# Optimization experiments

Hardware: AMD Instinct MI355X
Metric: run time of the kernel (lower is better)

## Reference

```python
import jax, jax.numpy as jnp
import numpy as np

N = 50000      # nodes (full graph: num_dst == num_src == N)
E = 800000     # edges, avg degree 16
D = 128        # in_feats == n_hidden == out_feats
L = 3          # n_layers
EPS = 1e-5     # BatchNorm1d eps


def setup_inputs() -> dict:
    key = jax.random.key(0)
    ks = jax.random.split(key, 6)
    feat = jax.random.normal(ks[0], (N, D), dtype=jnp.float32)
    src = jax.random.randint(ks[1], (E,), 0, N)
    dst = jax.random.randint(ks[2], (E,), 0, N)
    scale = 1.0 / np.sqrt(D)
    W_self = jax.random.normal(ks[3], (L, D, D), dtype=jnp.float32) * scale
    W_neigh = jax.random.normal(ks[4], (L, D, D), dtype=jnp.float32) * scale
    b = jax.random.normal(ks[5], (L, D), dtype=jnp.float32) * 0.01
    gamma = jnp.ones((L - 1, D), dtype=jnp.float32)
    beta = jnp.zeros((L - 1, D), dtype=jnp.float32)
    return {"feat": feat, "src": src, "dst": dst, "W_self": W_self,
            "W_neigh": W_neigh, "b": b, "gamma": gamma, "beta": beta}


def reference(feat, src, dst, W_self, W_neigh, b, gamma, beta):
    n = feat.shape[0]
    n_layers = W_self.shape[0]
    # in-degree of each dst node, clamped to 1 (zero-degree nodes aggregate 0)
    deg = jax.ops.segment_sum(jnp.ones_like(dst, dtype=feat.dtype), dst,
                              num_segments=n)
    deg = jnp.maximum(deg, 1.0)[:, None]                      # [N,1]
    h = feat
    for i in range(n_layers):
        # mean aggregation over incoming neighbors: gather + segment-sum
        agg = jax.ops.segment_sum(h[src], dst, num_segments=n) / deg  # [N,D]
        # SAGEConv('mean'): fc_self(h_dst) + fc_neigh(agg) + bias
        hn = h @ W_self[i] + agg @ W_neigh[i] + b[i]
        hn = hn + h                                           # residual (dims match)
        if i < n_layers - 1:
            mu = jnp.mean(hn, axis=0)
            var = jnp.var(hn, axis=0)                         # biased, as BN training
            hn = (hn - mu) * jax.lax.rsqrt(var + EPS) * gamma[i] + beta[i]
            hn = jax.nn.relu(hn)
        h = hn
    return h
```

## Files before the change

### kernel.cpp

```cpp
#include <hip/hip_runtime.h>

#define DIM 128
#define EPSF 1e-5f
#define BK_SHIFT 8
#define BK_NODES 256
#define GRP_SHIFT 13
#define NGRP 8
#define BKS_CAP 1536
#define MAXNBS 1600

typedef __attribute__((ext_vector_type(8))) short short8;
typedef __attribute__((ext_vector_type(4))) float float4v;

__device__ inline unsigned short f2bf(float x) {
    union { float f; unsigned u; } z; z.f = x;
    unsigned u = z.u;
    unsigned r = u + 0x7FFF + ((u >> 16) & 1);
    return (unsigned short)(r >> 16);
}
__device__ inline float bf2f(unsigned short u) {
    union { unsigned u; float f; } z; z.u = ((unsigned)u) << 16;
    return z.f;
}

__global__ void binA_kernel(const int* __restrict__ src, const int* __restrict__ dst,
                            unsigned* __restrict__ barr, int* __restrict__ bcnt,
                            int E, int NBS) {
    __shared__ int cnt[MAXNBS];
    __shared__ int gcur[MAXNBS];
    int tid = threadIdx.x;
    int tile0 = blockIdx.x * 4096;
    for (int j = tid; j < NBS; j += 256) cnt[j] = 0;
    __syncthreads();
    unsigned pk[16]; int bk[16];
#pragma unroll
    for (int i = 0; i < 16; ++i) {
        int e = tile0 + i * 256 + tid;
        if (e < E) {
            int d = dst[e];
            int s = src[e];
            bk[i] = ((d >> BK_SHIFT) << 3) | (s >> GRP_SHIFT);
            pk[i] = ((unsigned)(d & (BK_NODES - 1)) << 16) | (unsigned)s;
            atomicAdd(&cnt[bk[i]], 1);
        } else bk[i] = -1;
    }
    __syncthreads();
    for (int j = tid; j < NBS; j += 256) {
        int c = cnt[j];
        gcur[j] = (c > 0) ? atomicAdd(&bcnt[j], c) : 0;
    }
    __syncthreads();
#pragma unroll
    for (int i = 0; i < 16; ++i) {
        if (bk[i] >= 0) {
            int pos = atomicAdd(&gcur[bk[i]], 1);
            if (pos < BKS_CAP)
                barr[(size_t)bk[i] * BKS_CAP + pos] = pk[i];
        }
    }
}

__global__ void binB_kernel(const unsigned* __restrict__ barr, const int* __restrict__ bcnt,
                            int* __restrict__ rowptr, int* __restrict__ colidx,
                            int N, int E, int NBS) {
    __shared__ int hist[256];
    __shared__ int sm[256];
    __shared__ int bc[NGRP];
    int b = blockIdx.x;
    int tid = threadIdx.x;
    int lim = b * NGRP;
    int part = 0;
    for (int i = tid; i < lim; i += 256) part += bcnt[i];
    sm[tid] = part;
    if (tid < NGRP) bc[tid] = bcnt[lim + tid];
    __syncthreads();
    for (int off = 128; off > 0; off >>= 1) {
        if (tid < off) sm[tid] += sm[tid + off];
        __syncthreads();
    }
    int gb = sm[0];
    if (b == 0 && tid == 0) rowptr[N] = E;
    __syncthreads();
    hist[tid] = 0;
    __syncthreads();
    for (int g = 0; g < NGRP; ++g) {
        int cg = bc[g]; if (cg > BKS_CAP) cg = BKS_CAP;
        const unsigned* arr = barr + (size_t)(b * NGRP + g) * BKS_CAP;
        for (int i = tid; i < cg; i += 256)
            atomicAdd(&hist[arr[i] >> 16], 1);
    }
    __syncthreads();
    int h = hist[tid];
    sm[tid] = h;
    __syncthreads();
    for (int off = 1; off < 256; off <<= 1) {
        int x = (tid >= off) ? sm[tid - off] : 0;
        __syncthreads();
        sm[tid] += x;
        __syncthreads();
    }
    int base = sm[tid] - h;
    hist[tid] = base;
    int node = (b << BK_SHIFT) + tid;
    if (node < N) rowptr[node] = gb + base;
    __syncthreads();
    for (int g = 0; g < NGRP; ++g) {
        int cg = bc[g]; if (cg > BKS_CAP) cg = BKS_CAP;
        const unsigned* arr = barr + (size_t)(b * NGRP + g) * BKS_CAP;
        for (int i = tid; i < cg; i += 256) {
            unsigned u = arr[i];
            int pos = atomicAdd(&hist[u >> 16], 1);
            colidx[gb + pos] = (int)(u & 0xFFFFu);
        }
        __syncthreads();
    }
}

__global__ void prep_kernel(const float* __restrict__ Ws, const float* __restrict__ Wn,
                            unsigned short* __restrict__ wpack,
                            const float* __restrict__ feat, unsigned short* __restrict__ Hd,
                            int N) {
    int b = blockIdx.x;
    int tid = threadIdx.x;
    if (b < 24) {
        int l = b >> 3;
        int s = b & 7;
#pragma unroll
        for (int pi = 0; pi < 2; ++pi) {
            int p = tid * 2 + pi;
            int nt = p >> 6;
            int lane = p & 63;
            int kb = s * 32 + (lane >> 4) * 8;
            int col = nt * 16 + (lane & 15);
            unsigned short* dstp = wpack + (size_t)l * 32768 + ((size_t)(s * 8 + nt) * 64 + lane) * 8;
#pragma unroll
            for (int j = 0; j < 8; ++j) {
                int k = kb + j;
                float v = (k < 128) ? Ws[(size_t)l * 16384 + k * 128 + col]
                                    : Wn[(size_t)l * 16384 + (k - 128) * 128 + col];
                dstp[j] = f2bf(v);
            }
        }
        return;
    }
    int idx = (b - 24) * 256 + tid;
    if (idx >= N * 32) return;
    float4 v = ((const float4*)feat)[idx];
    ushort4 o;
    o.x = f2bf(v.x); o.y = f2bf(v.y); o.z = f2bf(v.z); o.w = f2bf(v.w);
    ((ushort4*)Hd)[idx] = o;
}

template<int BN>
__global__ void aggregate_kernel(const unsigned short* __restrict__ Hd,
                                 unsigned short* __restrict__ Acat,
                                 const int* __restrict__ rowptr,
                                 const int* __restrict__ colidx,
                                 const float* __restrict__ stats,
                                 const float* __restrict__ gamma,
                                 const float* __restrict__ beta,
                                 float invN, int N) {
    int wid = (blockIdx.x * blockDim.x + threadIdx.x) >> 6;
    if (wid >= N) return;
    int lane = threadIdx.x & 63;
    int half = lane >> 5, sl = lane & 31;
    float sc[4], sh[4];
    if (BN) {
#pragma unroll
        for (int j = 0; j < 4; ++j) {
            int c = sl * 4 + j;
            float mean = stats[c] * invN;
            float var = stats[128 + c] * invN - mean * mean;
            float s = gamma[c] * rsqrtf(var + EPSF);
            sc[j] = s; sh[j] = beta[c] - mean * s;
        }
    }
#define BNOP0(x) fmaxf(fmaf(bf2f(x), sc[0], sh[0]), 0.f)
#define BNOP1(x) fmaxf(fmaf(bf2f(x), sc[1], sh[1]), 0.f)
#define BNOP2(x) fmaxf(fmaf(bf2f(x), sc[2], sh[2]), 0.f)
#define BNOP3(x) fmaxf(fmaf(bf2f(x), sc[3], sh[3]), 0.f)
    int beg = rowptr[wid], end = rowptr[wid + 1];
    float4 acc = make_float4(0.f, 0.f, 0.f, 0.f);
    int e = beg + half;
    for (; e + 6 < end; e += 8) {
        int s0 = colidx[e];
        int s1 = colidx[e + 2];
        int s2 = colidx[e + 4];
        int s3 = colidx[e + 6];
        ushort4 u0 = *(const ushort4*)(Hd + (size_t)s0 * 128 + sl * 4);
        ushort4 u1 = *(const ushort4*)(Hd + (size_t)s1 * 128 + sl * 4);
        ushort4 u2 = *(const ushort4*)(Hd + (size_t)s2 * 128 + sl * 4);
        ushort4 u3 = *(const ushort4*)(Hd + (size_t)s3 * 128 + sl * 4);
        if (BN) {
            acc.x += (BNOP0(u0.x) + BNOP0(u1.x)) + (BNOP0(u2.x) + BNOP0(u3.x));
            acc.y += (BNOP1(u0.y) + BNOP1(u1.y)) + (BNOP1(u2.y) + BNOP1(u3.y));
            acc.z += (BNOP2(u0.z) + BNOP2(u1.z)) + (BNOP2(u2.z) + BNOP2(u3.z));
            acc.w += (BNOP3(u0.w) + BNOP3(u1.w)) + (BNOP3(u2.w) + BNOP3(u3.w));
        } else {
            acc.x += (bf2f(u0.x) + bf2f(u1.x)) + (bf2f(u2.x) + bf2f(u3.x));
            acc.y += (bf2f(u0.y) + bf2f(u1.y)) + (bf2f(u2.y) + bf2f(u3.y));
            acc.z += (bf2f(u0.z) + bf2f(u1.z)) + (bf2f(u2.z) + bf2f(u3.z));
            acc.w += (bf2f(u0.w) + bf2f(u1.w)) + (bf2f(u2.w) + bf2f(u3.w));
        }
    }
    for (; e < end; e += 2) {
        int s0 = colidx[e];
        ushort4 u0 = *(const ushort4*)(Hd + (size_t)s0 * 128 + sl * 4);
        if (BN) {
            acc.x += BNOP0(u0.x);
            acc.y += BNOP1(u0.y);
            acc.z += BNOP2(u0.z);
            acc.w += BNOP3(u0.w);
        } else {
            acc.x += bf2f(u0.x);
            acc.y += bf2f(u0.y);
            acc.z += bf2f(u0.z);
            acc.w += bf2f(u0.w);
        }
    }
    acc.x += __shfl_xor(acc.x, 32);
    acc.y += __shfl_xor(acc.y, 32);
    acc.z += __shfl_xor(acc.z, 32);
    acc.w += __shfl_xor(acc.w, 32);
    if (half == 0) {
        int deg = end - beg;
        float inv = 1.0f / (float)(deg > 0 ? deg : 1);
        ushort4 hrow = *(const ushort4*)(Hd + (size_t)wid * 128 + sl * 4);
        ushort4 ho;
        if (BN) {
            ho.x = f2bf(BNOP0(hrow.x));
            ho.y = f2bf(BNOP1(hrow.y));
            ho.z = f2bf(BNOP2(hrow.z));
            ho.w = f2bf(BNOP3(hrow.w));
        } else ho = hrow;
        *(ushort4*)(Acat + (size_t)wid * 256 + sl * 4) = ho;
        ushort4 o;
        o.x = f2bf(acc.x * inv); o.y = f2bf(acc.y * inv);
        o.z = f2bf(acc.z * inv); o.w = f2bf(acc.w * inv);
        *(ushort4*)(Acat + (size_t)wid * 256 + 128 + sl * 4) = o;
    }
#undef BNOP0
#undef BNOP1
#undef BNOP2
#undef BNOP3
}

__launch_bounds__(256)
__global__ void gemm_kernel(const unsigned short* __restrict__ Acat,
                            const unsigned short* __restrict__ wpack,
                            const float* __restrict__ bias,
                            unsigned short* __restrict__ outb, float* __restrict__ outf,
                            float* __restrict__ stats, int withStats, int N) {
    __shared__ unsigned short Bs[32768];
    int tid = threadIdx.x;
    {
        const float4* wsrc = (const float4*)wpack;
        float4* bdst = (float4*)Bs;
#pragma unroll
        for (int i = 0; i < 16; ++i) bdst[i * 256 + tid] = wsrc[i * 256 + tid];
    }
    __syncthreads();

    int wave = tid >> 6, lane = tid & 63;
    int row0 = blockIdx.x * 128 + wave * 32;
    int mrow = lane & 15, kq = lane >> 4;
    const unsigned short* Abase = Acat + (size_t)(row0 + mrow) * 256 + kq * 8;

    float4v acc[2][8];
#pragma unroll
    for (int i = 0; i < 2; ++i)
#pragma unroll
        for (int j = 0; j < 8; ++j) acc[i][j] = (float4v){0.f, 0.f, 0.f, 0.f};

#pragma unroll
    for (int s = 0; s < 8; ++s) {
        short8 a0 = *(const short8*)(Abase + s * 32);
        short8 a1 = *(const short8*)(Abase + 16 * 256 + s * 32);
#pragma unroll
        for (int nt = 0; nt < 8; ++nt) {
            short8 b = *(const short8*)(Bs + ((size_t)(s * 8 + nt) * 64 + lane) * 8);
            acc[0][nt] = __builtin_amdgcn_mfma_f32_16x16x32_bf16(a0, b, acc[0][nt], 0, 0, 0);
            acc[1][nt] = __builtin_amdgcn_mfma_f32_16x16x32_bf16(a1, b, acc[1][nt], 0, 0, 0);
        }
    }

    float* sm = (float*)Bs;
    if (withStats) {
        __syncthreads();
        sm[tid] = 0.f;
        __syncthreads();
    }

    int colb = lane & 15;
    int rq = (lane >> 4) * 4;
#pragma unroll
    for (int mt = 0; mt < 2; ++mt) {
        int rowt = row0 + mt * 16 + rq;
#pragma unroll
        for (int nt = 0; nt < 8; ++nt) {
            int col = nt * 16 + colb;
            float bv = bias[col];
            float slo = 0.f, qlo = 0.f;
#pragma unroll
            for (int r = 0; r < 4; ++r) {
                int row = rowt + r;
                if (row < N) {
                    float res = bf2f(Acat[(size_t)row * 256 + col]);
                    float v = acc[mt][nt][r] + bv + res;
                    if (withStats) {
                        outb[(size_t)row * 128 + col] = f2bf(v);
                        slo += v; qlo += v * v;
                    } else {
                        outf[(size_t)row * 128 + col] = v;
                    }
                }
            }
            if (withStats) {
                atomicAdd(&sm[col], slo);
                atomicAdd(&sm[128 + col], qlo);
            }
        }
    }
    if (withStats) {
        __syncthreads();
        if (tid < 128) {
            atomicAdd(&stats[tid], sm[tid]);
            atomicAdd(&stats[128 + tid], sm[128 + tid]);
        }
    }
}

extern "C" void kernel_launch(void* const* d_in, const int* in_sizes, int n_in,
                              void* d_out, int out_size, void* d_ws, size_t ws_size,
                              hipStream_t stream) {
    const float* feat  = (const float*)d_in[0];
    const int*   src   = (const int*)d_in[1];
    const int*   dst   = (const int*)d_in[2];
    const float* Wself = (const float*)d_in[3];
    const float* Wneig = (const float*)d_in[4];
    const float* bias  = (const float*)d_in[5];
    const float* gamma = (const float*)d_in[6];
    const float* beta  = (const float*)d_in[7];

    int N = in_sizes[0] / DIM;
    int E = in_sizes[1];
    int Npad = (N + 127) & ~127;
    int NB = (N + BK_NODES - 1) >> BK_SHIFT;
    int NBS = NB * NGRP;

    char* ws = (char*)d_ws;
    size_t off = 0;
    auto alloc = [&](size_t bytes) -> void* {
        void* p = ws + off;
        off = (off + bytes + 255) & ~(size_t)255;
        return p;
    };
    unsigned short* Acat   = (unsigned short*)alloc((size_t)Npad * 256 * 2);
    unsigned short* Hd     = (unsigned short*)alloc((size_t)Npad * 128 * 2);
    unsigned short* wpack  = (unsigned short*)alloc((size_t)3 * 32768 * 2);
    int*   colidx = (int*)alloc((size_t)E * 4);
    int*   rowptr = (int*)alloc((size_t)(N + 1) * 4);
    int*   bcnt   = (int*)alloc(MAXNBS * 4);
    float* stats  = (float*)alloc(512 * 4);

    unsigned* barr = (unsigned*)Acat;

    hipMemsetAsync(bcnt, 0, MAXNBS * 4 + 512 * 4, stream);
    binA_kernel<<<(E + 4095) / 4096, 256, 0, stream>>>(src, dst, barr, bcnt, E, NBS);
    binB_kernel<<<NB, 256, 0, stream>>>(barr, bcnt, rowptr, colidx, N, E, NBS);

    prep_kernel<<<24 + (N * 32 + 255) / 256, 256, 0, stream>>>(Wself, Wneig, wpack, feat, Hd, N);

    float invN = 1.0f / (float)N;
    int nagg = (N + 3) / 4;

    aggregate_kernel<0><<<nagg, 256, 0, stream>>>(Hd, Acat, rowptr, colidx,
                                                  stats, gamma, beta, invN, N);
    gemm_kernel<<<Npad / 128, 256, 0, stream>>>(Acat, wpack, bias, Hd, (float*)d_out,
                                                stats, 1, N);
    aggregate_kernel<1><<<nagg, 256, 0, stream>>>(Hd, Acat, rowptr, colidx,
                                                  stats, gamma, beta, invN, N);
    gemm_kernel<<<Npad / 128, 256, 0, stream>>>(Acat, wpack + 32768, bias + DIM, Hd,
                                                (float*)d_out, stats + 256, 1, N);
    aggregate_kernel<1><<<nagg, 256, 0, stream>>>(Hd, Acat, rowptr, colidx,
                                                  stats + 256, gamma + DIM, beta + DIM, invN, N);
    gemm_kernel<<<Npad / 128, 256, 0, stream>>>(Acat, wpack + 2 * 32768, bias + 2 * DIM, Hd,
                                                (float*)d_out, stats, 0, N);
}
```

Measured before the change: 325.5 us.

## Fuse all three layers into one persistent cooperative kernel with grid syncs

Replaces the six per-layer aggregate and GEMM launches with a single cooperative persistent kernel that loops over layers and separates phases with grid-wide syncs. BatchNorm+ReLU now runs as a separate elementwise pass that writes a normalized bf16 buffer, instead of being applied on every gathered neighbour. The GEMM reads self and aggregated features from two separate buffers rather than one concatenated array, and streams weights from global memory instead of staging them in LDS. This removes launch gaps and repeated per-edge BN arithmetic, but adds grid-sync costs, an extra full pass over H per layer, and lower occupancy under the persistent grid.

```diff
diff --git a/kernel.cpp b/kernel.cpp
--- a/kernel.cpp
+++ b/kernel.cpp
@@ -1,4 +1,7 @@
 #include <hip/hip_runtime.h>
+#include <hip/hip_cooperative_groups.h>
+
+namespace cg = cooperative_groups;
 
 #define DIM 128
 #define EPSF 1e-5f
@@ -118,7 +121,7 @@
 
 __global__ void prep_kernel(const float* __restrict__ Ws, const float* __restrict__ Wn,
                             unsigned short* __restrict__ wpack,
-                            const float* __restrict__ feat, unsigned short* __restrict__ Hd,
+                            const float* __restrict__ feat, unsigned short* __restrict__ Hb,
                             int N) {
     int b = blockIdx.x;
     int tid = threadIdx.x;
@@ -148,185 +151,176 @@
     float4 v = ((const float4*)feat)[idx];
     ushort4 o;
     o.x = f2bf(v.x); o.y = f2bf(v.y); o.z = f2bf(v.z); o.w = f2bf(v.w);
-    ((ushort4*)Hd)[idx] = o;
-}
-
-template<int BN>
-__global__ void aggregate_kernel(const unsigned short* __restrict__ Hd,
-                                 unsigned short* __restrict__ Acat,
-                                 const int* __restrict__ rowptr,
-                                 const int* __restrict__ colidx,
-                                 const float* __restrict__ stats,
-                                 const float* __restrict__ gamma,
-                                 const float* __restrict__ beta,
-                                 float invN, int N) {
-    int wid = (blockIdx.x * blockDim.x + threadIdx.x) >> 6;
-    if (wid >= N) return;
-    int lane = threadIdx.x & 63;
-    int half = lane >> 5, sl = lane & 31;
-    float sc[4], sh[4];
-    if (BN) {
-#pragma unroll
-        for (int j = 0; j < 4; ++j) {
-            int c = sl * 4 + j;
-            float mean = stats[c] * invN;
-            float var = stats[128 + c] * invN - mean * mean;
-            float s = gamma[c] * rsqrtf(var + EPSF);
-            sc[j] = s; sh[j] = beta[c] - mean * s;
-        }
-    }
-#define BNOP0(x) fmaxf(fmaf(bf2f(x), sc[0], sh[0]), 0.f)
-#define BNOP1(x) fmaxf(fmaf(bf2f(x), sc[1], sh[1]), 0.f)
-#define BNOP2(x) fmaxf(fmaf(bf2f(x), sc[2], sh[2]), 0.f)
-#define BNOP3(x) fmaxf(fmaf(bf2f(x), sc[3], sh[3]), 0.f)
-    int beg = rowptr[wid], end = rowptr[wid + 1];
-    float4 acc = make_float4(0.f, 0.f, 0.f, 0.f);
-    int e = beg + half;
-    for (; e + 6 < end; e += 8) {
-        int s0 = colidx[e];
-        int s1 = colidx[e + 2];
-        int s2 = colidx[e + 4];
-        int s3 = colidx[e + 6];
-        ushort4 u0 = *(const ushort4*)(Hd + (size_t)s0 * 128 + sl * 4);
-        ushort4 u1 = *(const ushort4*)(Hd + (size_t)s1 * 128 + sl * 4);
-        ushort4 u2 = *(const ushort4*)(Hd + (size_t)s2 * 128 + sl * 4);
-        ushort4 u3 = *(const ushort4*)(Hd + (size_t)s3 * 128 + sl * 4);
-        if (BN) {
-            acc.x += (BNOP0(u0.x) + BNOP0(u1.x)) + (BNOP0(u2.x) + BNOP0(u3.x));
-            acc.y += (BNOP1(u0.y) + BNOP1(u1.y)) + (BNOP1(u2.y) + BNOP1(u3.y));
-            acc.z += (BNOP2(u0.z) + BNOP2(u1.z)) + (BNOP2(u2.z) + BNOP2(u3.z));
-            acc.w += (BNOP3(u0.w) + BNOP3(u1.w)) + (BNOP3(u2.w) + BNOP3(u3.w));
-        } else {
-            acc.x += (bf2f(u0.x) + bf2f(u1.x)) + (bf2f(u2.x) + bf2f(u3.x));
-            acc.y += (bf2f(u0.y) + bf2f(u1.y)) + (bf2f(u2.y) + bf2f(u3.y));
-            acc.z += (bf2f(u0.z) + bf2f(u1.z)) + (bf2f(u2.z) + bf2f(u3.z));
-            acc.w += (bf2f(u0.w) + bf2f(u1.w)) + (bf2f(u2.w) + bf2f(u3.w));
-        }
-    }
-    for (; e < end; e += 2) {
-        int s0 = colidx[e];
-        ushort4 u0 = *(const ushort4*)(Hd + (size_t)s0 * 128 + sl * 4);
-        if (BN) {
-            acc.x += BNOP0(u0.x);
-            acc.y += BNOP1(u0.y);
-            acc.z += BNOP2(u0.z);
-            acc.w += BNOP3(u0.w);
-        } else {
-            acc.x += bf2f(u0.x);
-            acc.y += bf2f(u0.y);
-            acc.z += bf2f(u0.z);
-            acc.w += bf2f(u0.w);
-        }
-    }
-    acc.x += __shfl_xor(acc.x, 32);
-    acc.y += __shfl_xor(acc.y, 32);
-    acc.z += __shfl_xor(acc.z, 32);
-    acc.w += __shfl_xor(acc.w, 32);
-    if (half == 0) {
-        int deg = end - beg;
-        float inv = 1.0f / (float)(deg > 0 ? deg : 1);
-        ushort4 hrow = *(const ushort4*)(Hd + (size_t)wid * 128 + sl * 4);
-        ushort4 ho;
-        if (BN) {
-            ho.x = f2bf(BNOP0(hrow.x));
-            ho.y = f2bf(BNOP1(hrow.y));
-            ho.z = f2bf(BNOP2(hrow.z));
-            ho.w = f2bf(BNOP3(hrow.w));
-        } else ho = hrow;
-        *(ushort4*)(Acat + (size_t)wid * 256 + sl * 4) = ho;
-        ushort4 o;
-        o.x = f2bf(acc.x * inv); o.y = f2bf(acc.y * inv);
-        o.z = f2bf(acc.z * inv); o.w = f2bf(acc.w * inv);
-        *(ushort4*)(Acat + (size_t)wid * 256 + 128 + sl * 4) = o;
-    }
-#undef BNOP0
-#undef BNOP1
-#undef BNOP2
-#undef BNOP3
-}
-
-__launch_bounds__(256)
-__global__ void gemm_kernel(const unsigned short* __restrict__ Acat,
-                            const unsigned short* __restrict__ wpack,
-                            const float* __restrict__ bias,
-                            unsigned short* __restrict__ outb, float* __restrict__ outf,
-                            float* __restrict__ stats, int withStats, int N) {
-    __shared__ unsigned short Bs[32768];
-    int tid = threadIdx.x;
-    {
-        const float4* wsrc = (const float4*)wpack;
-        float4* bdst = (float4*)Bs;
-#pragma unroll
-        for (int i = 0; i < 16; ++i) bdst[i * 256 + tid] = wsrc[i * 256 + tid];
-    }
-    __syncthreads();
-
-    int wave = tid >> 6, lane = tid & 63;
-    int row0 = blockIdx.x * 128 + wave * 32;
-    int mrow = lane & 15, kq = lane >> 4;
-    const unsigned short* Abase = Acat + (size_t)(row0 + mrow) * 256 + kq * 8;
-
-    float4v acc[2][8];
-#pragma unroll
-    for (int i = 0; i < 2; ++i)
-#pragma unroll
-        for (int j = 0; j < 8; ++j) acc[i][j] = (float4v){0.f, 0.f, 0.f, 0.f};
-
-#pragma unroll
-    for (int s = 0; s < 8; ++s) {
-        short8 a0 = *(const short8*)(Abase + s * 32);
-        short8 a1 = *(const short8*)(Abase + 16 * 256 + s * 32);
-#pragma unroll
-        for (int nt = 0; nt < 8; ++nt) {
-            short8 b = *(const short8*)(Bs + ((size_t)(s * 8 + nt) * 64 + lane) * 8);
-            acc[0][nt] = __builtin_amdgcn_mfma_f32_16x16x32_bf16(a0, b, acc[0][nt], 0, 0, 0);
-            acc[1][nt] = __builtin_amdgcn_mfma_f32_16x16x32_bf16(a1, b, acc[1][nt], 0, 0, 0);
-        }
-    }
-
-    float* sm = (float*)Bs;
-    if (withStats) {
-        __syncthreads();
-        sm[tid] = 0.f;
-        __syncthreads();
-    }
-
-    int colb = lane & 15;
-    int rq = (lane >> 4) * 4;
-#pragma unroll
-    for (int mt = 0; mt < 2; ++mt) {
-        int rowt = row0 + mt * 16 + rq;
-#pragma unroll
-        for (int nt = 0; nt < 8; ++nt) {
-            int col = nt * 16 + colb;
-            float bv = bias[col];
-            float slo = 0.f, qlo = 0.f;
-#pragma unroll
-            for (int r = 0; r < 4; ++r) {
-                int row = rowt + r;
-                if (row < N) {
-                    float res = bf2f(Acat[(size_t)row * 256 + col]);
-                    float v = acc[mt][nt][r] + bv + res;
-                    if (withStats) {
-                        outb[(size_t)row * 128 + col] = f2bf(v);
-                        slo += v; qlo += v * v;
-                    } else {
-                        outf[(size_t)row * 128 + col] = v;
+    ((ushort4*)Hb)[idx] = o;
+}
+
+__launch_bounds__(256, 4)
+__global__ void layers_kernel(unsigned short* __restrict__ Hb,
+                              unsigned short* __restrict__ Agg,
+                              unsigned short* __restrict__ Hd,
+                              const int* __restrict__ rowptr,
+                              const int* __restrict__ colidx,
+                              const unsigned short* __restrict__ wpack,
+                              const float* __restrict__ bias,
+                              const float* __restrict__ gamma,
+                              const float* __restrict__ beta,
+                              float* __restrict__ stats,
+                              float* __restrict__ outf,
+                              float invN, int N, int Npad) {
+    cg::grid_group grid = cg::this_grid();
+    __shared__ float sm[256];
+    const int tid = threadIdx.x;
+    const int gthreads = gridDim.x * 256;
+    const int lane = tid & 63;
+
+    for (int l = 0; l < 3; ++l) {
+        if (l > 0) {
+            const volatile float* st = stats + (size_t)(l - 1) * 256;
+            int idx0 = blockIdx.x * 256 + tid;
+            int c0 = (idx0 & 31) * 4;
+            float sc[4], sh[4];
+#pragma unroll
+            for (int j = 0; j < 4; ++j) {
+                float mean = st[c0 + j] * invN;
+                float var = st[128 + c0 + j] * invN - mean * mean;
+                float s = gamma[(size_t)(l - 1) * DIM + c0 + j] * rsqrtf(var + EPSF);
+                sc[j] = s;
+                sh[j] = beta[(size_t)(l - 1) * DIM + c0 + j] - mean * s;
+            }
+            for (int idx = idx0; idx < N * 32; idx += gthreads) {
+                ushort4 u = ((const ushort4*)Hd)[idx];
+                ushort4 o;
+                o.x = f2bf(fmaxf(fmaf(bf2f(u.x), sc[0], sh[0]), 0.f));
+                o.y = f2bf(fmaxf(fmaf(bf2f(u.y), sc[1], sh[1]), 0.f));
+                o.z = f2bf(fmaxf(fmaf(bf2f(u.z), sc[2], sh[2]), 0.f));
+                o.w = f2bf(fmaxf(fmaf(bf2f(u.w), sc[3], sh[3]), 0.f));
+                ((ushort4*)Hb)[idx] = o;
+            }
+            grid.sync();
+        }
+
+        {
+            int gw = (blockIdx.x * 256 + tid) >> 6;
+            int nw = gthreads >> 6;
+            int half = lane >> 5, sl = lane & 31;
+            for (int wid = gw; wid < N; wid += nw) {
+                int beg = rowptr[wid], end = rowptr[wid + 1];
+                float4 acc = make_float4(0.f, 0.f, 0.f, 0.f);
+                int e = beg + half;
+                for (; e + 6 < end; e += 8) {
+                    int s0 = colidx[e];
+                    int s1 = colidx[e + 2];
+                    int s2 = colidx[e + 4];
+                    int s3 = colidx[e + 6];
+                    ushort4 u0 = *(const ushort4*)(Hb + (size_t)s0 * 128 + sl * 4);
+                    ushort4 u1 = *(const ushort4*)(Hb + (size_t)s1 * 128 + sl * 4);
+                    ushort4 u2 = *(const ushort4*)(Hb + (size_t)s2 * 128 + sl * 4);
+                    ushort4 u3 = *(const ushort4*)(Hb + (size_t)s3 * 128 + sl * 4);
+                    acc.x += (bf2f(u0.x) + bf2f(u1.x)) + (bf2f(u2.x) + bf2f(u3.x));
+                    acc.y += (bf2f(u0.y) + bf2f(u1.y)) + (bf2f(u2.y) + bf2f(u3.y));
+                    acc.z += (bf2f(u0.z) + bf2f(u1.z)) + (bf2f(u2.z) + bf2f(u3.z));
+                    acc.w += (bf2f(u0.w) + bf2f(u1.w)) + (bf2f(u2.w) + bf2f(u3.w));
+                }
+                for (; e < end; e += 2) {
+                    int s0 = colidx[e];
+                    ushort4 u0 = *(const ushort4*)(Hb + (size_t)s0 * 128 + sl * 4);
+                    acc.x += bf2f(u0.x);
+                    acc.y += bf2f(u0.y);
+                    acc.z += bf2f(u0.z);
+                    acc.w += bf2f(u0.w);
+                }
+                acc.x += __shfl_xor(acc.x, 32);
+                acc.y += __shfl_xor(acc.y, 32);
+                acc.z += __shfl_xor(acc.z, 32);
+                acc.w += __shfl_xor(acc.w, 32);
+                if (half == 0) {
+                    int deg = end - beg;
+                    float inv = 1.0f / (float)(deg > 0 ? deg : 1);
+                    ushort4 o;
+                    o.x = f2bf(acc.x * inv); o.y = f2bf(acc.y * inv);
+                    o.z = f2bf(acc.z * inv); o.w = f2bf(acc.w * inv);
+                    *(ushort4*)(Agg + (size_t)wid * 128 + sl * 4) = o;
+                }
+            }
+        }
+        grid.sync();
+
+        {
+            const unsigned short* wl = wpack + (size_t)l * 32768;
+            int withStats = (l < 2) ? 1 : 0;
+            int ntile = Npad >> 7;
+            int wave = tid >> 6;
+            int mrow = lane & 15, kq = lane >> 4;
+            for (int t = blockIdx.x; t < ntile; t += gridDim.x) {
+                int row0 = t * 128 + wave * 32;
+                const unsigned short* Sbase = Hb + (size_t)(row0 + mrow) * 128 + kq * 8;
+                const unsigned short* Gbase = Agg + (size_t)(row0 + mrow) * 128 + kq * 8;
+
+                float4v acc[2][8];
+#pragma unroll
+                for (int i = 0; i < 2; ++i)
+#pragma unroll
+                    for (int j = 0; j < 8; ++j) acc[i][j] = (float4v){0.f, 0.f, 0.f, 0.f};
+
+#pragma unroll
+                for (int s = 0; s < 8; ++s) {
+                    const unsigned short* ab = (s < 4) ? (Sbase + s * 32)
+                                                       : (Gbase + (s - 4) * 32);
+                    short8 a0 = *(const short8*)ab;
+                    short8 a1 = *(const short8*)(ab + 16 * 128);
+#pragma unroll
+                    for (int nt = 0; nt < 8; ++nt) {
+                        short8 b = *(const short8*)(wl + ((size_t)(s * 8 + nt) * 64 + lane) * 8);
+                        acc[0][nt] = __builtin_amdgcn_mfma_f32_16x16x32_bf16(a0, b, acc[0][nt], 0, 0, 0);
+                        acc[1][nt] = __builtin_amdgcn_mfma_f32_16x16x32_bf16(a1, b, acc[1][nt], 0, 0, 0);
                     }
                 }
-            }
-            if (withStats) {
-                atomicAdd(&sm[col], slo);
-                atomicAdd(&sm[128 + col], qlo);
-            }
-        }
-    }
-    if (withStats) {
-        __syncthreads();
-        if (tid < 128) {
-            atomicAdd(&stats[tid], sm[tid]);
-            atomicAdd(&stats[128 + tid], sm[128 + tid]);
-        }
+
+                if (withStats) {
+                    __syncthreads();
+                    sm[tid] = 0.f;
+                    __syncthreads();
+                }
+                int colb = lane & 15;
+                int rq = (lane >> 4) * 4;
+#pragma unroll
+                for (int mt = 0; mt < 2; ++mt) {
+                    int rowt = row0 + mt * 16 + rq;
+#pragma unroll
+                    for (int nt = 0; nt < 8; ++nt) {
+                        int col = nt * 16 + colb;
+                        float bv = bias[(size_t)l * DIM + col];
+                        float slo = 0.f, qlo = 0.f;
+#pragma unroll
+                        for (int r = 0; r < 4; ++r) {
+                            int row = rowt + r;
+                            if (row < N) {
+                                float res = bf2f(Hb[(size_t)row * 128 + col]);
+                                float v = acc[mt][nt][r] + bv + res;
+                                if (withStats) {
+                                    Hd[(size_t)row * 128 + col] = f2bf(v);
+                                    slo += v; qlo += v * v;
+                                } else {
+                                    outf[(size_t)row * 128 + col] = v;
+                                }
+                            }
+                        }
+                        if (withStats) {
+                            atomicAdd(&sm[col], slo);
+                            atomicAdd(&sm[128 + col], qlo);
+                        }
+                    }
+                }
+                if (withStats) {
+                    __syncthreads();
+                    if (tid < 128) {
+                        atomicAdd(&stats[(size_t)l * 256 + tid], sm[tid]);
+                        atomicAdd(&stats[(size_t)l * 256 + 128 + tid], sm[128 + tid]);
+                    }
+                }
+            }
+        }
+        if (l < 2) grid.sync();
     }
 }
 
@@ -355,35 +349,38 @@
         off = (off + bytes + 255) & ~(size_t)255;
         return p;
     };
-    unsigned short* Acat   = (unsigned short*)alloc((size_t)Npad * 256 * 2);
-    unsigned short* Hd     = (unsigned short*)alloc((size_t)Npad * 128 * 2);
-    unsigned short* wpack  = (unsigned short*)alloc((size_t)3 * 32768 * 2);
+    unsigned short* Hb    = (unsigned short*)alloc((size_t)Npad * 128 * 2);
+    unsigned short* Agg   = (unsigned short*)alloc((size_t)Npad * 128 * 2);
+    unsigned short* Hd    = (unsigned short*)alloc((size_t)Npad * 128 * 2);
+    unsigned short* wpack = (unsigned short*)alloc((size_t)3 * 32768 * 2);
     int*   colidx = (int*)alloc((size_t)E * 4);
     int*   rowptr = (int*)alloc((size_t)(N + 1) * 4);
     int*   bcnt   = (int*)alloc(MAXNBS * 4);
     float* stats  = (float*)alloc(512 * 4);
-
-    unsigned* barr = (unsigned*)Acat;
+    float* outf   = (float*)d_out;
+
+    unsigned* barr = (unsigned*)Agg;
 
     hipMemsetAsync(bcnt, 0, MAXNBS * 4 + 512 * 4, stream);
     binA_kernel<<<(E + 4095) / 4096, 256, 0, stream>>>(src, dst, barr, bcnt, E, NBS);
     binB_kernel<<<NB, 256, 0, stream>>>(barr, bcnt, rowptr, colidx, N, E, NBS);
 
-    prep_kernel<<<24 + (N * 32 + 255) / 256, 256, 0, stream>>>(Wself, Wneig, wpack, feat, Hd, N);
+    prep_kernel<<<24 + (N * 32 + 255) / 256, 256, 0, stream>>>(Wself, Wneig, wpack, feat, Hb, N);
 
     float invN = 1.0f / (float)N;
-    int nagg = (N + 3) / 4;
-
-    aggregate_kernel<0><<<nagg, 256, 0, stream>>>(Hd, Acat, rowptr, colidx,
-                                                  stats, gamma, beta, invN, N);
-    gemm_kernel<<<Npad / 128, 256, 0, stream>>>(Acat, wpack, bias, Hd, (float*)d_out,
-                                                stats, 1, N);
-    aggregate_kernel<1><<<nagg, 256, 0, stream>>>(Hd, Acat, rowptr, colidx,
-                                                  stats, gamma, beta, invN, N);
-    gemm_kernel<<<Npad / 128, 256, 0, stream>>>(Acat, wpack + 32768, bias + DIM, Hd,
-                                                (float*)d_out, stats + 256, 1, N);
-    aggregate_kernel<1><<<nagg, 256, 0, stream>>>(Hd, Acat, rowptr, colidx,
-                                                  stats + 256, gamma + DIM, beta + DIM, invN, N);
-    gemm_kernel<<<Npad / 128, 256, 0, stream>>>(Acat, wpack + 2 * 32768, bias + 2 * DIM, Hd,
-                                                (float*)d_out, stats, 0, N);
-}
+
+    static int coopGrid = 0;
+    if (coopGrid == 0) {
+        int numCU = 0, maxB = 0;
+        hipDeviceGetAttribute(&numCU, hipDeviceAttributeMultiprocessorCount, 0);
+        hipOccupancyMaxActiveBlocksPerMultiprocessor(&maxB, layers_kernel, 256, 0);
+        if (numCU <= 0) numCU = 256;
+        if (maxB <= 0) maxB = 2;
+        coopGrid = numCU * maxB;
+    }
+
+    void* args[] = { (void*)&Hb, (void*)&Agg, (void*)&Hd, (void*)&rowptr, (void*)&colidx,
+                     (void*)&wpack, (void*)&bias, (void*)&gamma, (void*)&beta,
+                     (void*)&stats, (void*)&outf, (void*)&invN, (void*)&N, (void*)&Npad };
+    hipLaunchCooperativeKernel(layers_kernel, dim3(coopGrid), dim3(256), args, 0, stream);
+}
```

New measurement: 1.013 ms. +211.1%, slower.
